# Kernel tuning notes

Measured on AMD Instinct MI355X. Metric: run time of the kernel, lower is better.

The kernel has to match this reference:

```python
import jax, jax.numpy as jnp
import numpy as np

SUPPORT = 7
NEIGHBOR = 10
EPS = 1e-12
BN_EPS = 1e-5


def knn(v, k):
    # v: (b, n, 3) -> (b, n, k) indices of k nearest (excluding self)
    sq = jnp.sum(v * v, -1)
    d = sq[:, :, None] + sq[:, None, :] - 2.0 * jnp.einsum('bnd,bmd->bnm', v, v)
    _, idx = jax.lax.top_k(-d, k + 1)
    return idx[:, :, 1:]


def gather_nb(f, idx):
    # f: (b, n, c), idx: (b, m, k) -> (b, m, k, c)
    b = f.shape[0]
    return f[jnp.arange(b)[:, None, None], idx]


def nb_dir_norm(v, idx):
    d = gather_nb(v, idx) - v[:, :, None, :]
    n = jnp.linalg.norm(d, axis=-1, keepdims=True)
    return d / jnp.maximum(n, EPS)


def norm0(d):
    n = jnp.linalg.norm(d, axis=0, keepdims=True)
    return d / jnp.maximum(n, EPS)


def conv_surface(idx, v, directions, kernel_num):
    b, n, k = idx.shape
    dn = nb_dir_norm(v, idx)
    theta = jax.nn.relu(jnp.einsum('bnkd,de->bnke', dn, norm0(directions)))
    theta = theta.reshape(b, n, k, SUPPORT, kernel_num)
    return jnp.sum(jnp.max(theta, axis=2), axis=2)  # (b, n, kernel_num)


def conv_layer(idx, v, fmap, w, bias, directions, out_ch):
    b, n, k = idx.shape
    dn = nb_dir_norm(v, idx)
    theta = jax.nn.relu(jnp.einsum('bnkd,de->bnke', dn, norm0(directions)))  # (b,n,k,s*o)
    fout = fmap @ w + bias  # (b, n, (s+1)*o)
    center = fout[..., :out_ch]
    supp = gather_nb(fout[..., out_ch:], idx)  # (b, n, k, s*o)
    act = (theta * supp).reshape(b, n, k, SUPPORT, out_ch)
    return center + jnp.sum(jnp.max(act, axis=2), axis=2)


def pool(v, f, rate, nbn, seed):
    b, n, _ = v.shape
    idx = knn(v, nbn)
    pf = jnp.max(gather_nb(f, idx), axis=2)
    m = n // rate
    samp = jax.random.permutation(jax.random.key(seed), n)[:m]
    return v[:, samp, :], pf[:, samp, :]


def nearest_idx(tgt, src):
    d = (jnp.sum(src * src, -1)[:, None, :] + jnp.sum(tgt * tgt, -1)[:, :, None]
         - 2.0 * jnp.einsum('btd,bsd->bts', tgt, src))
    return jnp.argmin(d, axis=-1)  # (b, nt)


def bn(x, g, b_, m, var):
    # per-channel over last dim (torch BN1d after transpose)
    return (x - m) / jnp.sqrt(var + BN_EPS) * g + b_


def setup_inputs() -> dict:
    key = jax.random.key(0)
    ks = jax.random.split(key, 32)
    bs, n = 4, 2048
    d = {}
    d['vertices'] = jax.random.normal(ks[0], (bs, n, 3), jnp.float32)
    d['rgb_f'] = jax.random.normal(ks[1], (bs, 32, n), jnp.float32)
    d['dir0'] = jax.random.normal(ks[2], (3, SUPPORT * 64), jnp.float32)
    def conv_params(i, cin, cout):
        s = 1.0 / np.sqrt(cin)
        w = jax.random.uniform(ks[i], (cin, (SUPPORT + 1) * cout), jnp.float32, -s, s)
        b = jax.random.uniform(ks[i + 1], ((SUPPORT + 1) * cout,), jnp.float32, -s, s)
        dr = jax.random.normal(ks[i + 2], (3, SUPPORT * cout), jnp.float32)
        return w, b, dr
    d['w1'], d['b1'], d['d1'] = conv_params(3, 128, 128)
    d['w2'], d['b2'], d['d2'] = conv_params(6, 128, 256)
    d['w3'], d['b3'], d['d3'] = conv_params(9, 256, 256)
    d['w4'], d['b4'], d['d4'] = conv_params(12, 256, 512)
    d['rgb_w'] = jax.random.normal(ks[15], (64, 32), jnp.float32) * 0.1
    d['rgb_b'] = jnp.zeros((64,), jnp.float32)
    for nm, c in [('rbn', 64), ('bn1', 128), ('bn2', 256), ('bn3', 256)]:
        d[nm + '_g'] = jnp.ones((c,), jnp.float32)
        d[nm + '_b'] = jnp.zeros((c,), jnp.float32)
        d[nm + '_m'] = jnp.zeros((c,), jnp.float32)
        d[nm + '_v'] = jnp.ones((c,), jnp.float32)
    return d


def reference(vertices, rgb_f, dir0,
              w1, b1, d1, w2, b2, d2, w3, b3, d3, w4, b4, d4,
              rgb_w, rgb_b,
              rbn_g, rbn_b, rbn_m, rbn_v,
              bn1_g, bn1_b, bn1_m, bn1_v,
              bn2_g, bn2_b, bn2_m, bn2_v,
              bn3_g, bn3_b, bn3_m, bn3_v):
    bs, n, _ = vertices.shape
    idx = knn(vertices, NEIGHBOR)
    fm0 = jax.nn.relu(conv_surface(idx, vertices, dir0, 64))  # (b, n, 64)
    # rgb_conv_1: Conv1d(32,64,1) -> ReLU -> BN
    rgb = jax.nn.relu(jnp.einsum('oc,bcn->bno', rgb_w, rgb_f) + rgb_b)  # (b, n, 64)
    rgb = bn(rgb, rbn_g, rbn_b, rbn_m, rbn_v)
    fm0 = jnp.concatenate([fm0, rgb], axis=-1)  # (b, n, 128)
    fm1 = jax.nn.relu(bn(conv_layer(idx, vertices, fm0, w1, b1, d1, 128),
                         bn1_g, bn1_b, bn1_m, bn1_v))
    v1, fp1 = pool(vertices, fm1, 4, 4, 1)  # (b, n/4, ...)
    k1 = min(NEIGHBOR, v1.shape[1] // 8)
    idx1 = knn(v1, k1)
    fm2 = jax.nn.relu(bn(conv_layer(idx1, v1, fp1, w2, b2, d2, 256),
                         bn2_g, bn2_b, bn2_m, bn2_v))
    fm3 = jax.nn.relu(bn(conv_layer(idx1, v1, fm2, w3, b3, d3, 256),
                         bn3_g, bn3_b, bn3_m, bn3_v))
    v2, fp2 = pool(v1, fm3, 4, 4, 2)  # (b, n/16, ...)
    k2 = min(NEIGHBOR, v2.shape[1] // 8)
    idx2 = knn(v2, k2)
    fm4 = conv_layer(idx2, v2, fp2, w4, b4, d4, 512)
    f_global = jnp.max(fm4, axis=1)  # (b, 512)
    ni1 = nearest_idx(vertices, v1)  # (b, n)
    ni2 = nearest_idx(vertices, v2)
    ar = jnp.arange(bs)[:, None]
    fm2u = fm2[ar, ni1]
    fm3u = fm3[ar, ni1]
    fm4u = fm4[ar, ni2]
    feat = jnp.concatenate([fm0, fm1, fm2u, fm3u, fm4u], axis=2)  # (b, n, 1280)
    fuse = jnp.concatenate([feat, jnp.broadcast_to(f_global[:, None, :], (bs, n, 512))], axis=2)
    return feat.transpose(0, 2, 1), fuse.transpose(0, 2, 1)
```

## Files before the change

### kernel.cpp

```cpp
#include <hip/hip_runtime.h>
#include <hip/hip_bf16.h>
#include <math.h>

#define NB 10
#define KNN_K 11

typedef __attribute__((ext_vector_type(8))) short bf16x8;
typedef __attribute__((ext_vector_type(4))) float f32x4;
typedef unsigned long long ull;

__device__ __forceinline__ float toF(float x) { return x; }
__device__ __forceinline__ float toF(__hip_bfloat16 x) { return __bfloat162float(x); }

__device__ __forceinline__ void tf2x32(unsigned k0, unsigned k1, unsigned& x0, unsigned& x1) {
  unsigned ks0 = k0, ks1 = k1, ks2 = k0 ^ k1 ^ 0x1BD11BDAu;
  x0 += ks0; x1 += ks1;
#define TF_R(r) { x0 += x1; x1 = (x1 << (r)) | (x1 >> (32 - (r))); x1 ^= x0; }
  TF_R(13) TF_R(15) TF_R(26) TF_R(6)  x0 += ks1; x1 += ks2 + 1u;
  TF_R(17) TF_R(29) TF_R(16) TF_R(24) x0 += ks2; x1 += ks0 + 2u;
  TF_R(13) TF_R(15) TF_R(26) TF_R(6)  x0 += ks0; x1 += ks1 + 3u;
  TF_R(17) TF_R(29) TF_R(16) TF_R(24) x0 += ks1; x1 += ks2 + 4u;
  TF_R(13) TF_R(15) TF_R(26) TF_R(6)  x0 += ks2; x1 += ks0 + 5u;
#undef TF_R
}

__device__ __forceinline__ void knn_wave_body(const float4* __restrict__ pts, int N, int qi,
                                              int lane, int* __restrict__ o) {
  float4 p = pts[qi];
  float bd[KNN_K]; int bi[KNN_K];
#pragma unroll
  for (int t = 0; t < KNN_K; ++t) { bd[t] = 3.4e38f; bi[t] = 0x7fffffff; }
  for (int j = lane; j < N; j += 64) {
    float4 q = pts[j];
    float dot = p.x * q.x + p.y * q.y + p.z * q.z;
    float d = p.w + q.w - 2.0f * dot;
    if (d < bd[KNN_K - 1]) {
      float cd = d; int ci = j;
#pragma unroll
      for (int t = 0; t < KNN_K; ++t) {
        bool sw = cd < bd[t];
        float td = bd[t]; int ti = bi[t];
        bd[t] = sw ? cd : td; bi[t] = sw ? ci : ti;
        cd = sw ? td : cd;   ci = sw ? ti : ci;
      }
    }
  }
  int ptr = 0;
#pragma unroll 1
  for (int t = 0; t < KNN_K; ++t) {
    float d = 3.4e38f; int idx = 0x7fffffff;
#pragma unroll
    for (int s = 0; s < KNN_K; ++s) {
      bool sel = (s == ptr);
      d = sel ? bd[s] : d;
      idx = sel ? bi[s] : idx;
    }
    float rd = d; int ridx = idx;
#pragma unroll
    for (int s = 32; s > 0; s >>= 1) {
      float od = __shfl_xor(rd, s);
      int oi = __shfl_xor(ridx, s);
      if (od < rd || (od == rd && oi < ridx)) { rd = od; ridx = oi; }
    }
    if (d == rd && idx == ridx) ptr++;
    if (t >= 1 && lane == 0) o[t - 1] = ridx;
  }
}

__global__ __launch_bounds__(1024) void setup_kernel(
    const float* __restrict__ w1, __hip_bfloat16* __restrict__ o1,
    const float* __restrict__ w2, __hip_bfloat16* __restrict__ o2,
    const float* __restrict__ w3, __hip_bfloat16* __restrict__ o3,
    const float* __restrict__ w4, __hip_bfloat16* __restrict__ o4,
    const float* __restrict__ s0, float* __restrict__ n0,
    const float* __restrict__ s1, float* __restrict__ n1,
    const float* __restrict__ s2, float* __restrict__ n2,
    const float* __restrict__ s3, float* __restrict__ n3,
    const float* __restrict__ s4, float* __restrict__ n4,
    int* __restrict__ p1a, int* __restrict__ p1b, int* __restrict__ samp2,
    const float* __restrict__ v, int* __restrict__ idx0) {
  __shared__ __align__(16) char smem[49152];
  int bid = blockIdx.x;
  if (bid < 480) {
    int sub = threadIdx.x >> 8, t = threadIdx.x & 255;
    int wtile = bid * 4 + sub;
    float (*tbuf)[33] = (float(*)[33])(smem + sub * (32 * 33 * 4));
    const float* W; __hip_bfloat16* O; int K, N;
    if (wtile < 128)      { W = w1; O = o1; K = 128; N = 1024; }
    else if (wtile < 384) { wtile -= 128; W = w2; O = o2; K = 128; N = 2048; }
    else if (wtile < 896) { wtile -= 384; W = w3; O = o3; K = 256; N = 2048; }
    else                  { wtile -= 896; W = w4; O = o4; K = 256; N = 4096; }
    int tpr = N / 32;
    int tk = wtile / tpr, tn = wtile % tpr;
    int tx = t & 31, ty = t >> 5;
#pragma unroll
    for (int i = 0; i < 4; ++i)
      tbuf[ty + 8 * i][tx] = W[(size_t)(tk * 32 + ty + 8 * i) * N + tn * 32 + tx];
    __syncthreads();
#pragma unroll
    for (int i = 0; i < 4; ++i)
      O[(size_t)(tn * 32 + ty + 8 * i) * K + tk * 32 + tx] = __float2bfloat16(tbuf[tx][ty + 8 * i]);
    return;
  }
  if (bid < 489) {
    int e = (bid - 480) * 1024 + threadIdx.x;
    const float* S; float* D; int W;
    if (e < 448)                          { S = s0; D = n0; W = 448; }
    else if (e < 448 + 896)               { e -= 448; S = s1; D = n1; W = 896; }
    else if (e < 448 + 896 + 1792)        { e -= 448 + 896; S = s2; D = n2; W = 1792; }
    else if (e < 448 + 896 + 3584)        { e -= 448 + 896 + 1792; S = s3; D = n3; W = 1792; }
    else if (e < 448 + 896 + 3584 + 3584) { e -= 448 + 896 + 3584; S = s4; D = n4; W = 3584; }
    else return;
    float a = S[e], b = S[W + e], c = S[2 * W + e];
    float nr = fmaxf(sqrtf(a * a + b * b + c * c), 1e-12f);
    D[e] = a / nr; D[W + e] = b / nr; D[2 * W + e] = c / nr;
    return;
  }
  if (bid < 506) {
    ull* keys = (ull*)smem;
    int which, chunk;
    if (bid < 497)      { which = 0; chunk = bid - 489; }
    else if (bid < 505) { which = 1; chunk = bid - 497; }
    else                { which = 2; chunk = 0; }
    unsigned mk0, mk1;
    if (which == 0)      { mk0 = 0u; mk1 = 1u; }
    else if (which == 1) { unsigned a0 = 0u, a1 = 0u; tf2x32(0u, 1u, a0, a1); mk0 = a0; mk1 = a1; }
    else                 { mk0 = 0u; mk1 = 2u; }
    unsigned sk0 = 0u, sk1 = 1u;
    tf2x32(mk0, mk1, sk0, sk1);
    int n = (which == 2) ? 512 : 2048;
    int* outp = (which == 0) ? p1a : (which == 1) ? p1b : samp2;
    for (int i = threadIdx.x; i < n; i += 1024) {
      unsigned y0 = 0u, y1 = (unsigned)i;
      tf2x32(sk0, sk1, y0, y1);
      keys[i] = ((ull)(y0 ^ y1) << 32) | (unsigned)i;
    }
    __syncthreads();
    int rpb = (which == 2) ? 512 : 256;
    int tpr = 1024 / rpb;
    int row = chunk * rpb + (int)(threadIdx.x / tpr);
    int sub = threadIdx.x % tpr;
    int seg = n / tpr;
    ull my = keys[row];
    int cnt = 0;
    for (int j = sub * seg; j < (sub + 1) * seg; ++j) cnt += (keys[j] < my) ? 1 : 0;
#pragma unroll
    for (int m = 1; m < 4; m <<= 1)
      if (m < tpr) cnt += __shfl_xor(cnt, m);
    if (sub == 0) outp[cnt] = row;
    return;
  }
  {
    float4* pts = (float4*)smem;
    int i = bid - 506;
    int b = i >> 7, x = i & 127;
    const int N = 2048;
    const float* vb = v + (size_t)b * N * 3;
    for (int i2 = threadIdx.x; i2 < N; i2 += 1024) {
      float xx = vb[i2 * 3], yy = vb[i2 * 3 + 1], zz = vb[i2 * 3 + 2];
      pts[i2] = make_float4(xx, yy, zz, xx * xx + yy * yy + zz * zz);
    }
    __syncthreads();
    int wave = threadIdx.x >> 6;
    int lane = threadIdx.x & 63;
    int qi = x * 16 + wave;
    knn_wave_body(pts, N, qi, lane, idx0 + ((size_t)b * N + qi) * NB);
  }
}

__global__ __launch_bounds__(1024) void knn_wave_kernel(const float* __restrict__ v, int N,
                                                        int* __restrict__ out) {
  __shared__ float4 pts[2048];
  int b = blockIdx.y;
  const float* vb = v + (size_t)b * N * 3;
  for (int i = threadIdx.x; i < N; i += blockDim.x) {
    float x = vb[i * 3], y = vb[i * 3 + 1], z = vb[i * 3 + 2];
    pts[i] = make_float4(x, y, z, x * x + y * y + z * z);
  }
  __syncthreads();
  int qpb = blockDim.x >> 6;
  int wave = threadIdx.x >> 6;
  int lane = threadIdx.x & 63;
  int qi = blockIdx.x * qpb + wave;
  knn_wave_body(pts, N, qi, lane, out + ((size_t)b * N + qi) * NB);
}

__global__ __launch_bounds__(256) void fm0n_kernel(const float* __restrict__ v, const int* __restrict__ idx,
                                                   const float* __restrict__ dir0n,
                                                   const float* __restrict__ rgb_f, const float* __restrict__ w,
                                                   const float* __restrict__ bias, const float* __restrict__ g,
                                                   const float* __restrict__ bb, const float* __restrict__ mm,
                                                   const float* __restrict__ vv,
                                                   const int* __restrict__ p1a, const int* __restrict__ p1b,
                                                   const int* __restrict__ samp2,
                                                   float* __restrict__ fm0, __hip_bfloat16* __restrict__ fm0b,
                                                   int* __restrict__ ni1, int* __restrict__ ni2) {
  int z = blockIdx.z;
  int b = blockIdx.y;
  int tid = threadIdx.x;
  if (z >= 1) {
    __shared__ float4 sp[512];
    int S = (z == 1) ? 512 : 128;
    int* outp = (z == 1) ? ni1 : ni2;
    for (int i = tid; i < S; i += blockDim.x) {
      int src = (z == 1) ? p1a[p1b[i]] : p1a[p1b[samp2[i]]];
      const float* q = v + ((size_t)b * 2048 + src) * 3;
      float x = q[0], y = q[1], zz = q[2];
      sp[i] = make_float4(x, y, zz, x * x + y * y + zz * zz);
    }
    __syncthreads();
    int wave = tid >> 6, lane = tid & 63;
    int n = blockIdx.x * 4 + wave;
    const float* t = v + ((size_t)b * 2048 + n) * 3;
    float x = t[0], y = t[1], zz = t[2];
    float sqt = x * x + y * y + zz * zz;
    float best = 3.4e38f; int bi = 0x7fffffff;
    for (int s = lane; s < S; s += 64) {
      float4 q = sp[s];
      float d = q.w + sqt - 2.f * (x * q.x + y * q.y + zz * q.z);
      if (d < best) { best = d; bi = s; }
    }
#pragma unroll
    for (int m = 32; m > 0; m >>= 1) {
      float od = __shfl_xor(best, m);
      int oi = __shfl_xor(bi, m);
      if (od < best || (od == best && oi < bi)) { best = od; bi = oi; }
    }
    if (lane == 0) outp[(size_t)b * 2048 + n] = bi;
    return;
  }
  __shared__ float dn[4][NB][3];
  int n0 = blockIdx.x * 4;
  if (tid < 4 * NB) {
    int p = tid / NB, k = tid % NB;
    size_t row = (size_t)b * 2048 + (n0 + p);
    const float* c = v + row * 3;
    int nb = idx[row * NB + k];
    const float* q = v + ((size_t)b * 2048 + nb) * 3;
    float dx = q[0] - c[0], dy = q[1] - c[1], dz = q[2] - c[2];
    float nr = fmaxf(sqrtf(dx * dx + dy * dy + dz * dz), 1e-12f);
    dn[p][k][0] = dx / nr; dn[p][k][1] = dy / nr; dn[p][k][2] = dz / nr;
  }
  __syncthreads();
  int p = tid >> 6, c = tid & 63;
  int n = n0 + p;
  float acc = 0.f;
  for (int s = 0; s < 7; ++s) {
    int e = s * 64 + c;
    float d0 = dir0n[e], d1 = dir0n[448 + e], d2 = dir0n[896 + e];
    float mx = 0.f;
#pragma unroll
    for (int k = 0; k < NB; ++k) {
      float t = dn[p][k][0] * d0 + dn[p][k][1] * d1 + dn[p][k][2] * d2;
      mx = fmaxf(mx, fmaxf(t, 0.f));
    }
    acc += mx;
  }
  acc = fmaxf(acc, 0.f);
  const float* f = rgb_f + (size_t)b * 32 * 2048;
  float a2 = bias[c];
  for (int cc = 0; cc < 32; ++cc) a2 += w[c * 32 + cc] * f[cc * 2048 + n];
  a2 = fmaxf(a2, 0.f);
  a2 = (a2 - mm[c]) / sqrtf(vv[c] + 1e-5f) * g[c] + bb[c];
  size_t o = ((size_t)b * 2048 + n) * 128;
  fm0[o + c] = acc;
  fm0[o + 64 + c] = a2;
  fm0b[o + c] = __float2bfloat16(acc);
  fm0b[o + 64 + c] = __float2bfloat16(a2);
}

__global__ __launch_bounds__(256) void mfma_gemm_kernel(const __hip_bfloat16* __restrict__ A,
                                                        const __hip_bfloat16* __restrict__ BT,
                                                        const float* __restrict__ bias,
                                                        float* __restrict__ C,
                                                        __hip_bfloat16* __restrict__ Cb,
                                                        int M, int K, int N) {
  __shared__ __hip_bfloat16 Al[128 * 32];
  __shared__ __hip_bfloat16 Bl[128 * 32];
  int t = threadIdx.x;
  int l = t & 63;
  int w = t >> 6;
  int wm = w >> 1, wn = w & 1;
  int m0 = blockIdx.y * 128, n0 = blockIdx.x * 128;
  f32x4 zero = {0.f, 0.f, 0.f, 0.f};
  f32x4 acc[4][4];
#pragma unroll
  for (int i = 0; i < 4; ++i)
#pragma unroll
    for (int j = 0; j < 4; ++j) acc[i][j] = zero;

  for (int kt = 0; kt < K; kt += 32) {
#pragma unroll
    for (int j = 0; j < 2; ++j) {
      int c = t + 256 * j;
      int r = c >> 2, o = c & 3;
      *(uint4*)&Al[r * 32 + o * 8] = *(const uint4*)&A[(size_t)(m0 + r) * K + kt + o * 8];
      *(uint4*)&Bl[r * 32 + o * 8] = *(const uint4*)&BT[(size_t)(n0 + r) * K + kt + o * 8];
    }
    __syncthreads();
    bf16x8 af[4], bfv[4];
#pragma unroll
    for (int f = 0; f < 4; ++f) {
      af[f]  = *(const bf16x8*)&Al[(wm * 64 + f * 16 + (l & 15)) * 32 + (l >> 4) * 8];
      bfv[f] = *(const bf16x8*)&Bl[(wn * 64 + f * 16 + (l & 15)) * 32 + (l >> 4) * 8];
    }
#pragma unroll
    for (int i = 0; i < 4; ++i)
#pragma unroll
      for (int j = 0; j < 4; ++j)
        acc[i][j] = __builtin_amdgcn_mfma_f32_16x16x32_bf16(af[i], bfv[j], acc[i][j], 0, 0, 0);
    __syncthreads();
  }
  int col_l = l & 15, rbase = (l >> 4) * 4;
#pragma unroll
  for (int i = 0; i < 4; ++i) {
#pragma unroll
    for (int j = 0; j < 4; ++j) {
      int col = n0 + wn * 64 + j * 16 + col_l;
      float bv = bias[col];
#pragma unroll
      for (int r = 0; r < 4; ++r) {
        int m = m0 + wm * 64 + i * 16 + rbase + r;
        float val = acc[i][j][r] + bv;
        if (C)  C[(size_t)m * N + col] = val;
        if (Cb) Cb[(size_t)m * N + col] = __float2bfloat16(val);
      }
    }
  }
}

template <typename T>
__global__ __launch_bounds__(256) void conv_combine3_kernel(
    const int* __restrict__ idx, const float* __restrict__ v,
    const T* __restrict__ fout, const float* __restrict__ dirn,
    const float* __restrict__ g, const float* __restrict__ bb,
    const float* __restrict__ mm, const float* __restrict__ vv,
    int use_bn_relu, float* __restrict__ outf, __hip_bfloat16* __restrict__ outb,
    int Np, int Cout) {
  __shared__ float dnS[2][NB][3];
  __shared__ int nbS[2][NB];
  int b = blockIdx.y;
  int tid = threadIdx.x;
  int base = blockIdx.x * 256;
  int p0 = base / Cout;
  int nPts = (Cout < 256) ? 2 : 1;
  if (tid < nPts * NB) {
    int p = tid / NB, k = tid - p * NB;
    size_t prow = (size_t)b * Np + p0 + p;
    int nb = idx[prow * NB + k];
    const float* cpt = v + prow * 3;
    const float* q = v + ((size_t)b * Np + nb) * 3;
    float dx = q[0] - cpt[0], dy = q[1] - cpt[1], dz = q[2] - cpt[2];
    float nr = fmaxf(sqrtf(dx * dx + dy * dy + dz * dz), 1e-12f);
    dnS[p][k][0] = dx / nr; dnS[p][k][1] = dy / nr; dnS[p][k][2] = dz / nr;
    nbS[p][k] = b * Np + nb;
  }
  __syncthreads();
  int gid = base + tid;
  int n = gid / Cout, c = gid - n * Cout;
  int lp = n - p0;
  size_t row = (size_t)b * Np + n;
  float dn0[NB], dn1[NB], dn2[NB]; int nbr[NB];
#pragma unroll
  for (int k = 0; k < NB; ++k) {
    dn0[k] = dnS[lp][k][0]; dn1[k] = dnS[lp][k][1]; dn2[k] = dnS[lp][k][2];
    nbr[k] = nbS[lp][k];
  }
  int F = 8 * Cout, W7 = 7 * Cout;
  float acc = toF(fout[row * (size_t)F + c]);
  for (int s = 0; s < 7; ++s) {
    int e = s * Cout + c;
    float d0 = dirn[e], d1 = dirn[W7 + e], d2 = dirn[2 * W7 + e];
    float mx = -3.4e38f;
#pragma unroll
    for (int k = 0; k < NB; ++k) {
      float t = fmaxf(dn0[k] * d0 + dn1[k] * d1 + dn2[k] * d2, 0.f);
      float sv = toF(fout[(size_t)nbr[k] * F + Cout + e]);
      mx = fmaxf(mx, t * sv);
    }
    acc += mx;
  }
  if (use_bn_relu) {
    acc = (acc - mm[c]) / sqrtf(vv[c] + 1e-5f) * g[c] + bb[c];
    acc = fmaxf(acc, 0.f);
  }
  outf[row * (size_t)Cout + c] = acc;
  if (outb) outb[row * (size_t)Cout + c] = __float2bfloat16(acc);
}

__global__ void pool_kernel(const float* __restrict__ v, const float* __restrict__ fm,
                            const int* __restrict__ idx10,
                            const int* __restrict__ sampA, const int* __restrict__ sampB,
                            float* __restrict__ v_out, float* __restrict__ f_out,
                            __hip_bfloat16* __restrict__ f_out_b, int Nin, int C) {
  int b = blockIdx.y, mi = blockIdx.x, c = threadIdx.x;
  int n = sampB ? sampA[sampB[mi]] : sampA[mi];
  size_t row = (size_t)b * Nin + n;
  float mx = -3.4e38f;
#pragma unroll
  for (int j = 0; j < 4; ++j) {
    int nb = idx10[row * NB + j];
    mx = fmaxf(mx, fm[((size_t)b * Nin + nb) * C + c]);
  }
  int Mout = gridDim.x;
  f_out[((size_t)b * Mout + mi) * C + c] = mx;
  f_out_b[((size_t)b * Mout + mi) * C + c] = __float2bfloat16(mx);
  if (c < 3) v_out[((size_t)b * Mout + mi) * 3 + c] = v[row * 3 + c];
}

__global__ __launch_bounds__(256) void output3_kernel(
    const float* __restrict__ fm0, const float* __restrict__ fm1,
    const float* __restrict__ fm2, const float* __restrict__ fm3,
    const float* __restrict__ fm4,
    const int* __restrict__ ni1, const int* __restrict__ ni2,
    float* __restrict__ out) {
  __shared__ float tile[64][33];
  __shared__ int srow[64];
  int b = blockIdx.z;
  int cc0 = blockIdx.y * 32;
  int n0 = blockIdx.x * 64;
  int tid = threadIdx.x;
  float* out0 = out;
  float* out1 = out + (size_t)4 * 1280 * 2048;
  if (cc0 >= 1280) {
    __shared__ float red[8][32];
    __shared__ float fgv[32];
    int coff = cc0 - 1280;
    int tx = tid & 31, ty = tid >> 5;
    float pm = -3.4e38f;
    for (int p = ty; p < 128; p += 8)
      pm = fmaxf(pm, fm4[((size_t)b * 128 + p) * 512 + coff + tx]);
    red[ty][tx] = pm;
    __syncthreads();
    if (tid < 32) {
      float m = red[0][tid];
#pragma unroll
      for (int r = 1; r < 8; ++r) m = fmaxf(m, red[r][tid]);
      fgv[tid] = m;
    }
    __syncthreads();
    int lx = tid & 63, ly = tid >> 6;
#pragma unroll
    for (int ci = 0; ci < 8; ++ci) {
      int cl = ly + 4 * ci;
      out1[((size_t)b * 1792 + cc0 + cl) * 2048 + n0 + lx] = fgv[cl];
    }
    return;
  }
  const float* P; int Cs, coff, mode;
  if (cc0 < 128)       { P = fm0; Cs = 128; coff = cc0;        mode = 0; }
  else if (cc0 < 256)  { P = fm1; Cs = 128; coff = cc0 - 128;  mode = 0; }
  else if (cc0 < 512)  { P = fm2; Cs = 256; coff = cc0 - 256;  mode = 1; }
  else if (cc0 < 768)  { P = fm3; Cs = 256; coff = cc0 - 512;  mode = 1; }
  else                 { P = fm4; Cs = 512; coff = cc0 - 768;  mode = 2; }
  if (tid < 64) {
    int n = n0 + tid;
    size_t r2 = (size_t)b * 2048 + n;
    int sr;
    if (mode == 0)      sr = b * 2048 + n;
    else if (mode == 1) sr = b * 512 + ni1[r2];
    else                sr = b * 128 + ni2[r2];
    srow[tid] = sr;
  }
  __syncthreads();
  int tx = tid & 31, ty = tid >> 5;
#pragma unroll
  for (int r = 0; r < 8; ++r) {
    int nl = ty + 8 * r;
    tile[nl][tx] = P[(size_t)srow[nl] * Cs + coff + tx];
  }
  __syncthreads();
  int lx = tid & 63, ly = tid >> 6;
#pragma unroll
  for (int ci = 0; ci < 8; ++ci) {
    int cl = ly + 4 * ci;
    int cc = cc0 + cl;
    float vv = tile[lx][cl];
    out1[((size_t)b * 1792 + cc) * 2048 + n0 + lx] = vv;
    out0[((size_t)b * 1280 + cc) * 2048 + n0 + lx] = vv;
  }
}

extern "C" void kernel_launch(void* const* d_in, const int* in_sizes, int n_in,
                              void* d_out, int out_size, void* d_ws, size_t ws_size,
                              hipStream_t stream) {
  (void)in_sizes; (void)n_in; (void)out_size; (void)ws_size;
  const float* vertices = (const float*)d_in[0];
  const float* rgb_f    = (const float*)d_in[1];
  const float* dir0     = (const float*)d_in[2];
  const float* w1 = (const float*)d_in[3],  *b1 = (const float*)d_in[4],  *d1 = (const float*)d_in[5];
  const float* w2 = (const float*)d_in[6],  *b2 = (const float*)d_in[7],  *d2 = (const float*)d_in[8];
  const float* w3 = (const float*)d_in[9],  *b3 = (const float*)d_in[10], *d3 = (const float*)d_in[11];
  const float* w4 = (const float*)d_in[12], *b4 = (const float*)d_in[13], *d4 = (const float*)d_in[14];
  const float* rgb_w = (const float*)d_in[15], *rgb_b = (const float*)d_in[16];
  const float* rbn_g = (const float*)d_in[17], *rbn_b = (const float*)d_in[18];
  const float* rbn_m = (const float*)d_in[19], *rbn_v = (const float*)d_in[20];
  const float* bn1_g = (const float*)d_in[21], *bn1_b = (const float*)d_in[22];
  const float* bn1_m = (const float*)d_in[23], *bn1_v = (const float*)d_in[24];
  const float* bn2_g = (const float*)d_in[25], *bn2_b = (const float*)d_in[26];
  const float* bn2_m = (const float*)d_in[27], *bn2_v = (const float*)d_in[28];
  const float* bn3_g = (const float*)d_in[29], *bn3_b = (const float*)d_in[30];
  const float* bn3_m = (const float*)d_in[31], *bn3_v = (const float*)d_in[32];
  float* out = (float*)d_out;

  char* ws = (char*)d_ws;
  size_t off = 0;
  auto alloc = [&](size_t bytes) -> void* {
    void* p = ws + off;
    off += (bytes + 255) & ~(size_t)255;
    return p;
  };
  int*   p1a   = (int*)alloc(2048 * 4);
  int*   p1b   = (int*)alloc(2048 * 4);
  int*   samp2 = (int*)alloc(512 * 4);
  int*   idx0  = (int*)alloc((size_t)4 * 2048 * NB * 4);
  int*   idx1  = (int*)alloc((size_t)4 * 512 * NB * 4);
  int*   idx2  = (int*)alloc((size_t)4 * 128 * NB * 4);
  float* fm0   = (float*)alloc((size_t)4 * 2048 * 128 * 4);
  float* fm1   = (float*)alloc((size_t)4 * 2048 * 128 * 4);
  float* fout  = (float*)alloc((size_t)4 * 2048 * 1024 * 4);
  __hip_bfloat16* foutb = (__hip_bfloat16*)alloc((size_t)4 * 2048 * 1024 * 2);
  float* v1    = (float*)alloc((size_t)4 * 512 * 3 * 4);
  float* fp1   = (float*)alloc((size_t)4 * 512 * 128 * 4);
  float* fm2   = (float*)alloc((size_t)4 * 512 * 256 * 4);
  float* fm3   = (float*)alloc((size_t)4 * 512 * 256 * 4);
  float* v2    = (float*)alloc((size_t)4 * 128 * 3 * 4);
  float* fp2   = (float*)alloc((size_t)4 * 128 * 256 * 4);
  float* fm4   = (float*)alloc((size_t)4 * 128 * 512 * 4);
  int*   ni1   = (int*)alloc((size_t)4 * 2048 * 4);
  int*   ni2   = (int*)alloc((size_t)4 * 2048 * 4);
  __hip_bfloat16* fm0b = (__hip_bfloat16*)alloc((size_t)4 * 2048 * 128 * 2);
  __hip_bfloat16* fp1b = (__hip_bfloat16*)alloc((size_t)4 * 512 * 128 * 2);
  __hip_bfloat16* fm2b = (__hip_bfloat16*)alloc((size_t)4 * 512 * 256 * 2);
  __hip_bfloat16* fp2b = (__hip_bfloat16*)alloc((size_t)4 * 128 * 256 * 2);
  __hip_bfloat16* wt1  = (__hip_bfloat16*)alloc((size_t)1024 * 128 * 2);
  __hip_bfloat16* wt2  = (__hip_bfloat16*)alloc((size_t)2048 * 128 * 2);
  __hip_bfloat16* wt3  = (__hip_bfloat16*)alloc((size_t)2048 * 256 * 2);
  __hip_bfloat16* wt4  = (__hip_bfloat16*)alloc((size_t)4096 * 256 * 2);
  float* d0n = (float*)alloc((size_t)3 * 448 * 4);
  float* d1n = (float*)alloc((size_t)3 * 896 * 4);
  float* d2n = (float*)alloc((size_t)3 * 1792 * 4);
  float* d3n = (float*)alloc((size_t)3 * 1792 * 4);
  float* d4n = (float*)alloc((size_t)3 * 3584 * 4);

  setup_kernel<<<1018, 1024, 0, stream>>>(w1, wt1, w2, wt2, w3, wt3, w4, wt4,
                                          dir0, d0n, d1, d1n, d2, d2n, d3, d3n, d4, d4n,
                                          p1a, p1b, samp2, vertices, idx0);

  fm0n_kernel<<<dim3(512, 4, 3), 256, 0, stream>>>(vertices, idx0, d0n, rgb_f, rgb_w, rgb_b,
                                                   rbn_g, rbn_b, rbn_m, rbn_v, p1a, p1b, samp2,
                                                   fm0, fm0b, ni1, ni2);

  mfma_gemm_kernel<<<dim3(1024 / 128, 8192 / 128), 256, 0, stream>>>(fm0b, wt1, b1, nullptr, foutb, 8192, 128, 1024);
  conv_combine3_kernel<__hip_bfloat16><<<dim3(2048 * 128 / 256, 4), 256, 0, stream>>>(idx0, vertices, foutb, d1n,
      bn1_g, bn1_b, bn1_m, bn1_v, 1, fm1, nullptr, 2048, 128);

  pool_kernel<<<dim3(512, 4), 128, 0, stream>>>(vertices, fm1, idx0, p1a, p1b, v1, fp1, fp1b, 2048, 128);
  knn_wave_kernel<<<dim3(512 / 4, 4), 256, 0, stream>>>(v1, 512, idx1);

  mfma_gemm_kernel<<<dim3(2048 / 128, 2048 / 128), 256, 0, stream>>>(fp1b, wt2, b2, nullptr, foutb, 2048, 128, 2048);
  conv_combine3_kernel<__hip_bfloat16><<<dim3(512 * 256 / 256, 4), 256, 0, stream>>>(idx1, v1, foutb, d2n,
      bn2_g, bn2_b, bn2_m, bn2_v, 1, fm2, fm2b, 512, 256);
  mfma_gemm_kernel<<<dim3(2048 / 128, 2048 / 128), 256, 0, stream>>>(fm2b, wt3, b3, nullptr, foutb, 2048, 256, 2048);
  conv_combine3_kernel<__hip_bfloat16><<<dim3(512 * 256 / 256, 4), 256, 0, stream>>>(idx1, v1, foutb, d3n,
      bn3_g, bn3_b, bn3_m, bn3_v, 1, fm3, nullptr, 512, 256);

  pool_kernel<<<dim3(128, 4), 256, 0, stream>>>(v1, fm3, idx1, samp2, nullptr, v2, fp2, fp2b, 512, 256);
  knn_wave_kernel<<<dim3(128 / 4, 4), 256, 0, stream>>>(v2, 128, idx2);

  mfma_gemm_kernel<<<dim3(4096 / 128, 512 / 128), 256, 0, stream>>>(fp2b, wt4, b4, fout, nullptr, 512, 256, 4096);
  conv_combine3_kernel<float><<<dim3(128 * 512 / 256, 4), 256, 0, stream>>>(idx2, v2, fout, d4n,
      nullptr, nullptr, nullptr, nullptr, 0, fm4, nullptr, 128, 512);

  output3_kernel<<<dim3(32, 56, 4), 256, 0, stream>>>(fm0, fm1, fm2, fm3, fm4, ni1, ni2, out);
}
```

Baseline: 247.8 us.

## Replace per-lane KNN insertion sort with register distances and iterative wave argmin

The KNN search no longer keeps a sorted top-11 list per lane. Each lane now holds all its candidate distances in registers, and the 11 winners are pulled out by repeated per-lane masked argmin followed by a wave shuffle reduction. The KNN step is also split out of the fused setup kernel into its own templated launch, which shrinks the setup kernel's shared memory. This removes the branchy insertion sort, at the cost of 11 full rescans of up to 32 register values per lane, more register pressure at NITER=32, and one extra kernel launch.

Result: no change. 252.6 us (+2.0%).

```diff
diff --git a/kernel.cpp b/kernel.cpp
--- a/kernel.cpp
+++ b/kernel.cpp
@@ -24,50 +24,60 @@
 #undef TF_R
 }
 
-__device__ __forceinline__ void knn_wave_body(const float4* __restrict__ pts, int N, int qi,
-                                              int lane, int* __restrict__ o) {
+template <int NITER>
+__device__ __forceinline__ void knn_extract_body(const float4* __restrict__ pts, int qi,
+                                                 int lane, int* __restrict__ o) {
   float4 p = pts[qi];
-  float bd[KNN_K]; int bi[KNN_K];
-#pragma unroll
-  for (int t = 0; t < KNN_K; ++t) { bd[t] = 3.4e38f; bi[t] = 0x7fffffff; }
-  for (int j = lane; j < N; j += 64) {
-    float4 q = pts[j];
+  float d[NITER];
+#pragma unroll
+  for (int i = 0; i < NITER; ++i) {
+    float4 q = pts[lane + 64 * i];
     float dot = p.x * q.x + p.y * q.y + p.z * q.z;
-    float d = p.w + q.w - 2.0f * dot;
-    if (d < bd[KNN_K - 1]) {
-      float cd = d; int ci = j;
-#pragma unroll
-      for (int t = 0; t < KNN_K; ++t) {
-        bool sw = cd < bd[t];
-        float td = bd[t]; int ti = bi[t];
-        bd[t] = sw ? cd : td; bi[t] = sw ? ci : ti;
-        cd = sw ? td : cd;   ci = sw ? ti : ci;
-      }
-    }
-  }
-  int ptr = 0;
+    d[i] = p.w + q.w - 2.0f * dot;
+  }
+  unsigned mask = 0u;
 #pragma unroll 1
   for (int t = 0; t < KNN_K; ++t) {
-    float d = 3.4e38f; int idx = 0x7fffffff;
-#pragma unroll
-    for (int s = 0; s < KNN_K; ++s) {
-      bool sel = (s == ptr);
-      d = sel ? bd[s] : d;
-      idx = sel ? bi[s] : idx;
-    }
-    float rd = d; int ridx = idx;
+    float bestd = 3.4e38f; int besti = 0x7fffffff;
+#pragma unroll
+    for (int i = 0; i < NITER; ++i) {
+      bool valid = ((mask >> i) & 1u) == 0u;
+      bool better = valid && (d[i] < bestd);
+      bestd = better ? d[i] : bestd;
+      besti = better ? (lane + 64 * i) : besti;
+    }
+    float rd = bestd; int ridx = besti;
 #pragma unroll
     for (int s = 32; s > 0; s >>= 1) {
       float od = __shfl_xor(rd, s);
       int oi = __shfl_xor(ridx, s);
       if (od < rd || (od == rd && oi < ridx)) { rd = od; ridx = oi; }
     }
-    if (d == rd && idx == ridx) ptr++;
+    if ((ridx & 63) == lane) mask |= 1u << (ridx >> 6);
     if (t >= 1 && lane == 0) o[t - 1] = ridx;
   }
 }
 
-__global__ __launch_bounds__(1024) void setup_kernel(
+template <int NITER>
+__global__ __launch_bounds__(1024) void knn_wave_kernel(const float* __restrict__ v,
+                                                        int* __restrict__ out) {
+  __shared__ float4 pts[NITER * 64];
+  const int N = NITER * 64;
+  int b = blockIdx.y;
+  const float* vb = v + (size_t)b * N * 3;
+  for (int i = threadIdx.x; i < N; i += blockDim.x) {
+    float x = vb[i * 3], y = vb[i * 3 + 1], z = vb[i * 3 + 2];
+    pts[i] = make_float4(x, y, z, x * x + y * y + z * z);
+  }
+  __syncthreads();
+  int qpb = blockDim.x >> 6;
+  int wave = threadIdx.x >> 6;
+  int lane = threadIdx.x & 63;
+  int qi = blockIdx.x * qpb + wave;
+  knn_extract_body<NITER>(pts, qi, lane, out + ((size_t)b * N + qi) * NB);
+}
+
+__global__ __launch_bounds__(1024) void prep_kernel(
     const float* __restrict__ w1, __hip_bfloat16* __restrict__ o1,
     const float* __restrict__ w2, __hip_bfloat16* __restrict__ o2,
     const float* __restrict__ w3, __hip_bfloat16* __restrict__ o3,
@@ -77,9 +87,8 @@
     const float* __restrict__ s2, float* __restrict__ n2,
     const float* __restrict__ s3, float* __restrict__ n3,
     const float* __restrict__ s4, float* __restrict__ n4,
-    int* __restrict__ p1a, int* __restrict__ p1b, int* __restrict__ samp2,
-    const float* __restrict__ v, int* __restrict__ idx0) {
-  __shared__ __align__(16) char smem[49152];
+    int* __restrict__ p1a, int* __restrict__ p1b, int* __restrict__ samp2) {
+  __shared__ __align__(16) char smem[16896];
   int bid = blockIdx.x;
   if (bid < 480) {
     int sub = threadIdx.x >> 8, t = threadIdx.x & 255;
@@ -116,7 +125,7 @@
     D[e] = a / nr; D[W + e] = b / nr; D[2 * W + e] = c / nr;
     return;
   }
-  if (bid < 506) {
+  {
     ull* keys = (ull*)smem;
     int which, chunk;
     if (bid < 497)      { which = 0; chunk = bid - 489; }
@@ -148,41 +157,7 @@
     for (int m = 1; m < 4; m <<= 1)
       if (m < tpr) cnt += __shfl_xor(cnt, m);
     if (sub == 0) outp[cnt] = row;
-    return;
-  }
-  {
-    float4* pts = (float4*)smem;
-    int i = bid - 506;
-    int b = i >> 7, x = i & 127;
-    const int N = 2048;
-    const float* vb = v + (size_t)b * N * 3;
-    for (int i2 = threadIdx.x; i2 < N; i2 += 1024) {
-      float xx = vb[i2 * 3], yy = vb[i2 * 3 + 1], zz = vb[i2 * 3 + 2];
-      pts[i2] = make_float4(xx, yy, zz, xx * xx + yy * yy + zz * zz);
-    }
-    __syncthreads();
-    int wave = threadIdx.x >> 6;
-    int lane = threadIdx.x & 63;
-    int qi = x * 16 + wave;
-    knn_wave_body(pts, N, qi, lane, idx0 + ((size_t)b * N + qi) * NB);
-  }
-}
-
-__global__ __launch_bounds__(1024) void knn_wave_kernel(const float* __restrict__ v, int N,
-                                                        int* __restrict__ out) {
-  __shared__ float4 pts[2048];
-  int b = blockIdx.y;
-  const float* vb = v + (size_t)b * N * 3;
-  for (int i = threadIdx.x; i < N; i += blockDim.x) {
-    float x = vb[i * 3], y = vb[i * 3 + 1], z = vb[i * 3 + 2];
-    pts[i] = make_float4(x, y, z, x * x + y * y + z * z);
-  }
-  __syncthreads();
-  int qpb = blockDim.x >> 6;
-  int wave = threadIdx.x >> 6;
-  int lane = threadIdx.x & 63;
-  int qi = blockIdx.x * qpb + wave;
-  knn_wave_body(pts, N, qi, lane, out + ((size_t)b * N + qi) * NB);
+  }
 }
 
 __global__ __launch_bounds__(256) void fm0n_kernel(const float* __restrict__ v, const int* __restrict__ idx,
@@ -543,9 +518,11 @@
   float* d3n = (float*)alloc((size_t)3 * 1792 * 4);
   float* d4n = (float*)alloc((size_t)3 * 3584 * 4);
 
-  setup_kernel<<<1018, 1024, 0, stream>>>(w1, wt1, w2, wt2, w3, wt3, w4, wt4,
-                                          dir0, d0n, d1, d1n, d2, d2n, d3, d3n, d4, d4n,
-                                          p1a, p1b, samp2, vertices, idx0);
+  prep_kernel<<<506, 1024, 0, stream>>>(w1, wt1, w2, wt2, w3, wt3, w4, wt4,
+                                        dir0, d0n, d1, d1n, d2, d2n, d3, d3n, d4, d4n,
+                                        p1a, p1b, samp2);
+
+  knn_wave_kernel<32><<<dim3(128, 4), 1024, 0, stream>>>(vertices, idx0);
 
   fm0n_kernel<<<dim3(512, 4, 3), 256, 0, stream>>>(vertices, idx0, d0n, rgb_f, rgb_w, rgb_b,
                                                    rbn_g, rbn_b, rbn_m, rbn_v, p1a, p1b, samp2,
@@ -556,7 +533,7 @@
       bn1_g, bn1_b, bn1_m, bn1_v, 1, fm1, nullptr, 2048, 128);
 
   pool_kernel<<<dim3(512, 4), 128, 0, stream>>>(vertices, fm1, idx0, p1a, p1b, v1, fp1, fp1b, 2048, 128);
-  knn_wave_kernel<<<dim3(512 / 4, 4), 256, 0, stream>>>(v1, 512, idx1);
+  knn_wave_kernel<8><<<dim3(128, 4), 256, 0, stream>>>(v1, idx1);
 
   mfma_gemm_kernel<<<dim3(2048 / 128, 2048 / 128), 256, 0, stream>>>(fp1b, wt2, b2, nullptr, foutb, 2048, 128, 2048);
   conv_combine3_kernel<__hip_bfloat16><<<dim3(512 * 256 / 256, 4), 256, 0, stream>>>(idx1, v1, foutb, d2n,
@@ -566,7 +543,7 @@
       bn3_g, bn3_b, bn3_m, bn3_v, 1, fm3, nullptr, 512, 256);
 
   pool_kernel<<<dim3(128, 4), 256, 0, stream>>>(v1, fm3, idx1, samp2, nullptr, v2, fp2, fp2b, 512, 256);
-  knn_wave_kernel<<<dim3(128 / 4, 4), 256, 0, stream>>>(v2, 128, idx2);
+  knn_wave_kernel<2><<<dim3(32, 4), 256, 0, stream>>>(v2, idx2);
 
   mfma_gemm_kernel<<<dim3(4096 / 128, 512 / 128), 256, 0, stream>>>(fp2b, wt4, b4, fout, nullptr, 512, 256, 4096);
   conv_combine3_kernel<float><<<dim3(128 * 512 / 256, 4), 256, 0, stream>>>(idx2, v2, fout, d4n,
```
